# Kernel optimization log

Hardware: AMD Instinct MI355X
Metric: run time of the kernel (lower is better)

## Reference

```python
import jax, jax.numpy as jnp
import numpy as np

B, S, D = 4, 2048, 1024
H, DQK, DV = 16, 20, 64
DLQ, DLKV = 256, 128
EPS = 1e-6
NEG = -1e9


def _rms(x, w, eps=EPS):
    return x * jax.lax.rsqrt(jnp.mean(x * x, axis=-1, keepdims=True) + eps) * w


def setup_inputs() -> dict:
    key = jax.random.key(0)
    ks = jax.random.split(key, 12)
    sd = lambda n: 1.0 / np.sqrt(n)
    inp = {
        'h': jax.random.normal(ks[0], (B, S, D), jnp.float32),
        'mask': jnp.where(jnp.tril(jnp.ones((S, S), bool)), 0.0, NEG).astype(jnp.float32),
        'wq_a_w': jax.random.normal(ks[1], (DLQ, D), jnp.float32) * sd(D),
        'wq_a_b': jnp.zeros((DLQ,), jnp.float32),
        'q_norm_w': jnp.ones((DLQ,), jnp.float32),
        'wq_b_w': jax.random.normal(ks[2], (H * DQK, DLQ), jnp.float32) * sd(DLQ),
        'wq_b_b': jnp.zeros((H * DQK,), jnp.float32),
        'wkv_a_w': jax.random.normal(ks[3], (DLKV, D), jnp.float32) * sd(D),
        'wkv_a_b': jnp.zeros((DLKV,), jnp.float32),
        'kv_norm_w': jnp.ones((DLKV,), jnp.float32),
        'wkv_b_w': jax.random.normal(ks[4], (H * (DQK + DV), DLKV), jnp.float32) * sd(DLKV),
        'wo_w': jax.random.normal(ks[5], (D, H * DV), jnp.float32) * sd(H * DV),
        'wo_b': jnp.zeros((D,), jnp.float32),
    }
    return inp


def reference(h, mask, wq_a_w, wq_a_b, q_norm_w, wq_b_w, wq_b_b,
              wkv_a_w, wkv_a_b, kv_norm_w, wkv_b_w, wo_w, wo_b):
    b, s, _ = h.shape
    # query path: wq_b(q_norm(wq_a(h)))
    q_lat = _rms(h @ wq_a_w.T + wq_a_b, q_norm_w)
    q = (q_lat @ wq_b_w.T + wq_b_b).reshape(b, s, H, DQK)
    # latent kv (prefill, start_pos=0 => cache[:end_pos] == kv_norm of this chunk)
    kvn = _rms(h @ wkv_a_w.T + wkv_a_b, kv_norm_w)  # [b, t, c]
    wkv_b = wkv_b_w.reshape(H, DQK + DV, DLKV)
    # absorbed QK: project query into latent space
    q_kv = jnp.einsum('bshq,hqc->bshc', q, wkv_b[:, :DQK])
    scores = jnp.einsum('bshc,btc->bsht', q_kv, kvn) * (DQK ** -0.5)
    scores = scores + mask[:, None, :]  # causal, broadcast over heads
    p = jax.nn.softmax(scores, axis=-1).astype(h.dtype)
    v_lat = jnp.einsum('bsht,btc->bshc', p, kvn)
    v = jnp.einsum('bshc,hvc->bshv', v_lat, wkv_b[:, DQK:])
    return v.reshape(b, s, H * DV) @ wo_w.T + wo_b
```

## Files before the change

### kernel.cpp

```cpp
#include <hip/hip_runtime.h>
#include <stdint.h>

#define NB 4
#define SEQ 2048
#define DM 1024
#define NH 16
#define NDQK 20
#define NDV 64
#define DLQ 256
#define DLKV 128
#define MR (NB*SEQ)
#define NKV (NH*DLKV)

typedef __attribute__((ext_vector_type(8))) short bf8;
typedef __attribute__((ext_vector_type(4))) float f4;
typedef __attribute__((ext_vector_type(4))) short s4;

#define MFMA16(a,b,c) __builtin_amdgcn_mfma_f32_16x16x32_bf16(a, b, c, 0, 0, 0)

__device__ __forceinline__ short f2b(float f) {
  union { float f; unsigned u; } v; v.f = f;
  return (short)((v.u + 0x7FFFu + ((v.u >> 16) & 1u)) >> 16);
}

__device__ __forceinline__ void gld16(void* lds, const void* g) {
  __builtin_amdgcn_global_load_lds((const __attribute__((address_space(1))) void*)g,
                                   (__attribute__((address_space(3))) void*)lds, 16, 0, 0);
}

__global__ __launch_bounds__(256) void k_conv(const float* __restrict__ h,
    const float* __restrict__ wqa, const float* __restrict__ wkva,
    short* __restrict__ hb, short* __restrict__ wqab, short* __restrict__ wkvab) {
  const int NH4 = (MR*DM)/4, NQ4 = (DLQ*DM)/4, NK4 = (DLKV*DM)/4;
  int stride = gridDim.x * blockDim.x;
  for (int i = blockIdx.x*blockDim.x + threadIdx.x; i < NH4+NQ4+NK4; i += stride) {
    const float4* s; short* d; int o;
    if (i < NH4)            { s = (const float4*)h;    d = hb;     o = i; }
    else if (i < NH4+NQ4)   { s = (const float4*)wqa;  d = wqab;   o = i - NH4; }
    else                    { s = (const float4*)wkva; d = wkvab;  o = i - NH4 - NQ4; }
    float4 v = s[o];
    s4 r; r.x = f2b(v.x); r.y = f2b(v.y); r.z = f2b(v.z); r.w = f2b(v.w);
    *(s4*)(d + (size_t)o*4) = r;
  }
}

__global__ __launch_bounds__(256) void k_wcomb(const float* __restrict__ wqbw,
    const float* __restrict__ wqbb, const float* __restrict__ wkvb,
    short* __restrict__ Wc, float* __restrict__ bc) {
  const float SC = 0.22360679774997896f * 1.4426950408889634f;
  int n = blockIdx.x, l = threadIdx.x;
  int hh = n >> 7, c = n & 127;
  float acc = 0.f, bacc = 0.f;
  for (int q = 0; q < NDQK; ++q) {
    float wv = wkvb[(hh*84 + q)*128 + c];
    acc  += wqbw[(hh*20 + q)*256 + l] * wv;
    bacc += wqbb[hh*20 + q] * wv;
  }
  Wc[(size_t)n*256 + l] = f2b(acc * SC);
  if (l == 0) bc[n] = bacc * SC;
}

__global__ __launch_bounds__(256) void k_w2(const float* __restrict__ wo,
    const float* __restrict__ wkvb, short* __restrict__ W2) {
  int idx = blockIdx.x*256 + threadIdx.x;
  int d = idx >> 11, k = idx & 2047, hh = k >> 7, c = k & 127;
  float acc = 0.f;
  #pragma unroll 8
  for (int v = 0; v < NDV; ++v)
    acc += wo[d*1024 + hh*64 + v] * wkvb[(hh*84 + 20 + v)*128 + c];
  W2[idx] = f2b(acc);
}

template<int BN, bool WT>
__global__ __launch_bounds__(256) void k_proj_rms(const short* __restrict__ Ab,
    const short* __restrict__ Wb, const float* __restrict__ bias,
    const float* __restrict__ nw, short* __restrict__ outp, short* __restrict__ outT) {
  constexpr int WN = BN/4, NI = WN/16;
  __shared__ __align__(16) char As[32*128];
  __shared__ __align__(16) char Ws[BN*128];
  __shared__ float red[32][4];
  const int tid = threadIdx.x, l = tid & 63, w = tid >> 6;
  const int l15 = l & 15, l4 = l >> 4, l7 = l & 7, l3 = l >> 3;
  const int m0 = blockIdx.x * 32;
  f4 z = {0.f,0.f,0.f,0.f};
  f4 acc[2][NI];
  for (int mi=0;mi<2;mi++) for (int ni=0;ni<NI;ni++) acc[mi][ni] = z;
  for (int kt = 0; kt < DM/64; ++kt) {
    __syncthreads();
    { int row = w*8 + l3;
      gld16(As + w*1024 + l*16,
            (const char*)Ab + ((size_t)(m0+row)*DM + kt*64)*2 + ((l7 ^ (row&7))*16)); }
    #pragma unroll
    for (int i = 0; i < BN/32; ++i) {
      int ci = w*(BN/32) + i, row = ci*8 + l3;
      gld16(Ws + ci*1024 + l*16,
            (const char*)Wb + ((size_t)row*DM + kt*64)*2 + ((l7 ^ (row&7))*16));
    }
    asm volatile("s_waitcnt vmcnt(0)" ::: "memory");
    __syncthreads();
    #pragma unroll
    for (int kk = 0; kk < 2; ++kk) {
      bf8 a[2], bb[NI];
      #pragma unroll
      for (int mi=0;mi<2;mi++) { int row = mi*16 + l15;
        a[mi] = *(const bf8*)(As + row*128 + ((kk*64 + l4*16) ^ ((row&7)<<4))); }
      #pragma unroll
      for (int ni=0;ni<NI;ni++) { int n = w*WN + ni*16 + l15;
        bb[ni] = *(const bf8*)(Ws + n*128 + ((kk*64 + l4*16) ^ ((n&7)<<4))); }
      #pragma unroll
      for (int mi=0;mi<2;mi++)
        #pragma unroll
        for (int ni=0;ni<NI;ni++) acc[mi][ni] = MFMA16(a[mi], bb[ni], acc[mi][ni]);
    }
  }
  float bn[NI], nwv[NI];
  #pragma unroll
  for (int ni=0;ni<NI;ni++) { int n = w*WN + ni*16 + l15; bn[ni] = bias[n]; nwv[ni] = nw[n]; }
  #pragma unroll
  for (int mi=0;mi<2;mi++) {
    f4 v = z;
    #pragma unroll
    for (int ni=0;ni<NI;ni++)
      #pragma unroll
      for (int r=0;r<4;r++) { acc[mi][ni][r] += bn[ni]; v[r] += acc[mi][ni][r]*acc[mi][ni][r]; }
    #pragma unroll
    for (int r=0;r<4;r++)
      for (int x=1;x<16;x<<=1) v[r] += __shfl_xor(v[r], x);
    if (l15 == 0) {
      #pragma unroll
      for (int r=0;r<4;r++) red[mi*16 + l4*4 + r][w] = v[r];
    }
  }
  __syncthreads();
  #pragma unroll
  for (int mi=0;mi<2;mi++) {
    float sc[4];
    #pragma unroll
    for (int r=0;r<4;r++) { int row = mi*16 + l4*4 + r;
      float t = red[row][0] + red[row][1] + red[row][2] + red[row][3];
      sc[r] = rsqrtf(t * (1.0f/BN) + 1e-6f); }
    #pragma unroll
    for (int ni=0;ni<NI;ni++) { int n = w*WN + ni*16 + l15;
      #pragma unroll
      for (int r=0;r<4;r++) {
        int m = m0 + mi*16 + l4*4 + r;
        short bv = f2b(acc[mi][ni][r] * sc[r] * nwv[ni]);
        outp[(size_t)m*BN + n] = bv;
        if (WT) { int bb2 = m >> 11, s = m & 2047;
                  outT[((size_t)bb2*DLKV + n)*SEQ + s] = bv; }
      }
    }
  }
}

template<bool BOUT>
__global__ __launch_bounds__(256) void k_gemm(const short* __restrict__ A,
    const short* __restrict__ W, const float* __restrict__ bias,
    void* __restrict__ outp, int N, int K) {
  __shared__ __align__(16) char As[128*128];
  __shared__ __align__(16) char Ws[128*128];
  const int tid = threadIdx.x, l = tid & 63, w = tid >> 6;
  const int l15 = l&15, l4 = l>>4, l7 = l&7, l3 = l>>3;
  const int wm = w >> 1, wn = w & 1;
  const int n0 = blockIdx.x * 128, m0 = blockIdx.y * 128;
  f4 z = {0.f,0.f,0.f,0.f};
  f4 acc[4][4];
  for (int mi=0;mi<4;mi++) for (int ni=0;ni<4;ni++) acc[mi][ni] = z;
  for (int kt = 0; kt < (K>>6); ++kt) {
    __syncthreads();
    #pragma unroll
    for (int i=0;i<4;i++) {
      int ci = w*4 + i, row = ci*8 + l3;
      gld16(As + ci*1024 + l*16,
            (const char*)A + ((size_t)(m0+row)*K + kt*64)*2 + ((l7^(row&7))*16));
      gld16(Ws + ci*1024 + l*16,
            (const char*)W + ((size_t)(n0+row)*K + kt*64)*2 + ((l7^(row&7))*16));
    }
    asm volatile("s_waitcnt vmcnt(0)" ::: "memory");
    __syncthreads();
    #pragma unroll
    for (int kk=0;kk<2;kk++) {
      bf8 a[4], bb[4];
      #pragma unroll
      for (int mi=0;mi<4;mi++) { int row = wm*64+mi*16+l15;
        a[mi] = *(const bf8*)(As + row*128 + ((kk*64+l4*16)^((row&7)<<4))); }
      #pragma unroll
      for (int ni=0;ni<4;ni++) { int row = wn*64+ni*16+l15;
        bb[ni] = *(const bf8*)(Ws + row*128 + ((kk*64+l4*16)^((row&7)<<4))); }
      #pragma unroll
      for (int mi=0;mi<4;mi++)
        #pragma unroll
        for (int ni=0;ni<4;ni++) acc[mi][ni] = MFMA16(a[mi], bb[ni], acc[mi][ni]);
    }
  }
  #pragma unroll
  for (int ni=0;ni<4;ni++) {
    int n = n0 + wn*64 + ni*16 + l15;
    float bn = bias[n];
    #pragma unroll
    for (int mi=0;mi<4;mi++)
      #pragma unroll
      for (int r=0;r<4;r++) {
        int m = m0 + wm*64 + mi*16 + l4*4 + r;
        float val = acc[mi][ni][r] + bn;
        if (BOUT) ((short*)outp)[(size_t)m*N + n] = f2b(val);
        else      ((float*)outp)[(size_t)m*N + n] = val;
      }
  }
}

__global__ __launch_bounds__(64, 2) void k_flash(const short* __restrict__ qkv,
    const short* __restrict__ kvn, const short* __restrict__ kvnT,
    short* __restrict__ vlat) {
  __shared__ __align__(16) short Pl[32*72];
  const int l = threadIdx.x & 63;
  const int l15 = l & 15, l4 = l >> 4;
  const int hb = blockIdx.x, hh = hb & 15, b = hb >> 4;
  const int qb = 63 - (int)blockIdx.y;
  const int qw = qb * 32;
  const size_t rowbase = (size_t)(b*SEQ + qw);
  const short* Kbase = kvn  + (size_t)b*SEQ*DLKV;
  const short* Vbase = kvnT + (size_t)b*DLKV*SEQ;

  bf8 qf[2][4];
  #pragma unroll
  for (int mi=0;mi<2;mi++)
    #pragma unroll
    for (int kk=0;kk<4;kk++)
      qf[mi][kk] = *(const bf8*)(qkv + (rowbase + mi*16 + l15)*NKV + hh*128 + kk*32 + l4*8);

  f4 z = {0.f,0.f,0.f,0.f};
  f4 acc[2][8], sums[2]; float mr[2][4];
  #pragma unroll
  for (int mi=0;mi<2;mi++) { sums[mi] = z;
    #pragma unroll
    for (int cf=0;cf<8;cf++) acc[mi][cf] = z;
    #pragma unroll
    for (int r=0;r<4;r++) mr[mi][r] = -3.0e38f; }

  const short ONE = 0x3F80;
  bf8 ones; 
  #pragma unroll
  for (int j=0;j<8;j++) ones[j] = ONE;

  const int nt = ((qw + 31) >> 6) + 1;
  for (int it = 0; it < nt; ++it) {
    const int t0 = it*64;
    f4 sc[2][4];
    #pragma unroll
    for (int mi=0;mi<2;mi++)
      #pragma unroll
      for (int tf=0;tf<4;tf++) sc[mi][tf] = z;
    #pragma unroll
    for (int kk=0;kk<4;kk++) {
      bf8 bk[4];
      #pragma unroll
      for (int tf=0;tf<4;tf++)
        bk[tf] = *(const bf8*)(Kbase + (size_t)(t0 + tf*16 + l15)*DLKV + kk*32 + l4*8);
      #pragma unroll
      for (int mi=0;mi<2;mi++)
        #pragma unroll
        for (int tf=0;tf<4;tf++) sc[mi][tf] = MFMA16(qf[mi][kk], bk[tf], sc[mi][tf]);
    }
    if (t0 + 63 > qw) {
      #pragma unroll
      for (int mi=0;mi<2;mi++)
        #pragma unroll
        for (int tf=0;tf<4;tf++)
          #pragma unroll
          for (int r=0;r<4;r++) {
            int qg = qw + mi*16 + l4*4 + r, tg = t0 + tf*16 + l15;
            if (tg > qg) sc[mi][tf][r] = -3.0e38f;
          }
    }
    #pragma unroll
    for (int mi=0;mi<2;mi++) {
      float mn[4], al[4];
      #pragma unroll
      for (int r=0;r<4;r++) {
        float v = fmaxf(fmaxf(sc[mi][0][r], sc[mi][1][r]), fmaxf(sc[mi][2][r], sc[mi][3][r]));
        for (int x=1;x<16;x<<=1) v = fmaxf(v, __shfl_xor(v, x));
        float m2 = fmaxf(mr[mi][r], v);
        al[r] = exp2f(mr[mi][r] - m2);
        mr[mi][r] = m2; mn[r] = m2;
      }
      #pragma unroll
      for (int r=0;r<4;r++) { sums[mi][r] *= al[r];
        #pragma unroll
        for (int cf=0;cf<8;cf++) acc[mi][cf][r] *= al[r]; }
      #pragma unroll
      for (int tf=0;tf<4;tf++)
        #pragma unroll
        for (int r=0;r<4;r++)
          Pl[(mi*16 + l4*4 + r)*72 + tf*16 + l15] = f2b(exp2f(sc[mi][tf][r] - mn[r]));
    }
    #pragma unroll
    for (int kk=0;kk<2;kk++) {
      bf8 pa[2];
      #pragma unroll
      for (int mi=0;mi<2;mi++)
        pa[mi] = *(const bf8*)(Pl + (mi*16 + l15)*72 + kk*32 + l4*8);
      #pragma unroll
      for (int mi=0;mi<2;mi++) sums[mi] = MFMA16(pa[mi], ones, sums[mi]);
      #pragma unroll
      for (int cf=0;cf<8;cf++) {
        bf8 bv = *(const bf8*)(Vbase + (size_t)(cf*16 + l15)*SEQ + t0 + kk*32 + l4*8);
        #pragma unroll
        for (int mi=0;mi<2;mi++) acc[mi][cf] = MFMA16(pa[mi], bv, acc[mi][cf]);
      }
    }
  }
  #pragma unroll
  for (int mi=0;mi<2;mi++) {
    float inv[4];
    #pragma unroll
    for (int r=0;r<4;r++) inv[r] = 1.0f / sums[mi][r];
    #pragma unroll
    for (int cf=0;cf<8;cf++)
      #pragma unroll
      for (int r=0;r<4;r++) {
        size_t m = rowbase + mi*16 + l4*4 + r;
        vlat[m*NKV + hh*128 + cf*16 + l15] = f2b(acc[mi][cf][r] * inv[r]);
      }
  }
}

extern "C" void kernel_launch(void* const* d_in, const int* in_sizes, int n_in,
                              void* d_out, int out_size, void* d_ws, size_t ws_size,
                              hipStream_t stream) {
  const float* h     = (const float*)d_in[0];
  const float* wqaw  = (const float*)d_in[2];
  const float* wqa_b = (const float*)d_in[3];
  const float* qnw   = (const float*)d_in[4];
  const float* wqbw  = (const float*)d_in[5];
  const float* wqbb  = (const float*)d_in[6];
  const float* wkvaw = (const float*)d_in[7];
  const float* wkva_b= (const float*)d_in[8];
  const float* kvnw  = (const float*)d_in[9];
  const float* wkvb  = (const float*)d_in[10];
  const float* wow   = (const float*)d_in[11];
  const float* wob   = (const float*)d_in[12];

  char* ws = (char*)d_ws;
  size_t off = 0;
  auto alloc = [&](size_t bytes) { char* p = ws + off; off += (bytes + 255) & ~(size_t)255; return p; };
  short* hb     = (short*)alloc((size_t)MR*DM*2);
  short* wqab16 = (short*)alloc((size_t)DLQ*DM*2);
  short* wkvab16= (short*)alloc((size_t)DLKV*DM*2);
  short* qlat   = (short*)alloc((size_t)MR*DLQ*2);
  short* kvnb   = (short*)alloc((size_t)MR*DLKV*2);
  short* kvnT   = (short*)alloc((size_t)MR*DLKV*2);
  short* Wc     = (short*)alloc((size_t)NKV*DLQ*2);
  float* bc     = (float*)alloc((size_t)NKV*4);
  short* qkv    = (short*)alloc((size_t)MR*NKV*2);
  short* vlat   = (short*)alloc((size_t)MR*NKV*2);
  short* W2     = (short*)alloc((size_t)DM*NKV*2);

  k_conv<<<2048, 256, 0, stream>>>(h, wqaw, wkvaw, hb, wqab16, wkvab16);
  k_wcomb<<<NKV, 256, 0, stream>>>(wqbw, wqbb, wkvb, Wc, bc);
  k_w2<<<(DM*NKV)/256, 256, 0, stream>>>(wow, wkvb, W2);
  k_proj_rms<DLQ,  false><<<MR/32, 256, 0, stream>>>(hb, wqab16,  wqa_b,  qnw,  qlat, nullptr);
  k_proj_rms<DLKV, true ><<<MR/32, 256, 0, stream>>>(hb, wkvab16, wkva_b, kvnw, kvnb, kvnT);
  k_gemm<true ><<<dim3(NKV/128, MR/128), 256, 0, stream>>>(qlat, Wc, bc, qkv, NKV, DLQ);
  k_flash<<<dim3(64, 64), 64, 0, stream>>>(qkv, kvnb, kvnT, vlat);
  k_gemm<false><<<dim3(DM/128, MR/128), 256, 0, stream>>>(vlat, W2, wob, d_out, DM, NKV);
}
```

Baseline: 497.8 us.

## Restructure flash kernel: 8 heads per block share LDS K tiles, paired causal blocks

The flash-attention kernel now runs 8 waves per block, one per head, and all of them share one K tile of the latent KV. That tile is double-buffered in swizzled LDS through global_load_lds. Each block handles a short and a long causal query block (y and 63-y) back to back to balance work, and launches a flat grid of 256 blocks. It also prefetches V rows into registers ahead of the PV MFMAs and swaps the shuffle max reduction for DPP row operations. The aim is to cut redundant global K reads across heads and reduce load imbalance, at the cost of block-wide barriers and one block per CU.

```diff
diff --git a/kernel.cpp b/kernel.cpp
--- a/kernel.cpp
+++ b/kernel.cpp
@@ -26,6 +26,15 @@
 __device__ __forceinline__ void gld16(void* lds, const void* g) {
   __builtin_amdgcn_global_load_lds((const __attribute__((address_space(1))) void*)g,
                                    (__attribute__((address_space(3))) void*)lds, 16, 0, 0);
+}
+
+__device__ __forceinline__ float dppmax16(float v) {
+  int t;
+  t = __builtin_amdgcn_update_dpp(0, __float_as_int(v), 0xB1,  0xF, 0xF, true); v = fmaxf(v, __int_as_float(t));
+  t = __builtin_amdgcn_update_dpp(0, __float_as_int(v), 0x4E,  0xF, 0xF, true); v = fmaxf(v, __int_as_float(t));
+  t = __builtin_amdgcn_update_dpp(0, __float_as_int(v), 0x141, 0xF, 0xF, true); v = fmaxf(v, __int_as_float(t));
+  t = __builtin_amdgcn_update_dpp(0, __float_as_int(v), 0x140, 0xF, 0xF, true); v = fmaxf(v, __int_as_float(t));
+  return v;
 }
 
 __global__ __launch_bounds__(256) void k_conv(const float* __restrict__ h,
@@ -209,43 +218,65 @@
   }
 }
 
-__global__ __launch_bounds__(64, 2) void k_flash(const short* __restrict__ qkv,
+__global__ __launch_bounds__(512, 1) void k_flash(const short* __restrict__ qkv,
     const short* __restrict__ kvn, const short* __restrict__ kvnT,
     short* __restrict__ vlat) {
-  __shared__ __align__(16) short Pl[32*72];
-  const int l = threadIdx.x & 63;
+  __shared__ __align__(16) char Ks[2][64*256];
+  __shared__ __align__(16) short Pl[8][32*72];
+  const int tid = threadIdx.x, l = tid & 63, w = tid >> 6;
   const int l15 = l & 15, l4 = l >> 4;
-  const int hb = blockIdx.x, hh = hb & 15, b = hb >> 4;
-  const int qb = 63 - (int)blockIdx.y;
-  const int qw = qb * 32;
-  const size_t rowbase = (size_t)(b*SEQ + qw);
-  const short* Kbase = kvn  + (size_t)b*SEQ*DLKV;
-  const short* Vbase = kvnT + (size_t)b*DLKV*SEQ;
-
+  const int id = blockIdx.x;
+  const int b   = (id & 7) >> 1;
+  const int hh  = (((id >> 3) & 1) << 3) | w;
+  const int y   = ((id >> 4) << 1) | (id & 1);
+  const int qbs0 = y, qbs1 = 63 - y;
+  const int ntA = (y >> 1) + 1, ntT = 33;
+  const short* Kb = kvn  + (size_t)b*SEQ*DLKV;
+  const short* Vb = kvnT + (size_t)b*DLKV*SEQ;
+  short* Pw = Pl[w];
+
+  const short ONE = 0x3F80;
+  bf8 ones;
+  #pragma unroll
+  for (int j2=0;j2<8;j2++) ones[j2] = ONE;
+  f4 z = {0.f,0.f,0.f,0.f};
+
+  int qw = qbs0*32;
+  size_t rowbase = (size_t)b*SEQ + qw;
   bf8 qf[2][4];
-  #pragma unroll
-  for (int mi=0;mi<2;mi++)
+  f4 acc[2][8], sums[2]; float mr[2][4];
+  #pragma unroll
+  for (int mi=0;mi<2;mi++) {
     #pragma unroll
     for (int kk=0;kk<4;kk++)
       qf[mi][kk] = *(const bf8*)(qkv + (rowbase + mi*16 + l15)*NKV + hh*128 + kk*32 + l4*8);
-
-  f4 z = {0.f,0.f,0.f,0.f};
-  f4 acc[2][8], sums[2]; float mr[2][4];
-  #pragma unroll
-  for (int mi=0;mi<2;mi++) { sums[mi] = z;
+    sums[mi] = z;
     #pragma unroll
     for (int cf=0;cf<8;cf++) acc[mi][cf] = z;
     #pragma unroll
-    for (int r=0;r<4;r++) mr[mi][r] = -3.0e38f; }
-
-  const short ONE = 0x3F80;
-  bf8 ones; 
-  #pragma unroll
-  for (int j=0;j<8;j++) ones[j] = ONE;
-
-  const int nt = ((qw + 31) >> 6) + 1;
-  for (int it = 0; it < nt; ++it) {
-    const int t0 = it*64;
+    for (int r=0;r<4;r++) mr[mi][r] = -3.0e38f;
+  }
+
+  #pragma unroll
+  for (int r=0;r<2;r++) {
+    int ci = r*512 + tid, row = ci >> 4, c16 = ci & 15;
+    gld16(Ks[0] + ci*16, (const char*)Kb + row*256 + ((c16 ^ (row & 7))*16));
+  }
+  int cur = 0, t = 0;
+  for (int j = 0; j < ntT; ++j) {
+    const int tn = (j+1 >= ntT) ? t : ((j+1 == ntA) ? 0 : t+1);
+    {
+      const char* src = (const char*)(Kb + (size_t)tn*64*DLKV);
+      #pragma unroll
+      for (int r=0;r<2;r++) {
+        int ci = r*512 + tid, row = ci >> 4, c16 = ci & 15;
+        gld16(Ks[cur^1] + ci*16, src + row*256 + ((c16 ^ (row & 7))*16));
+      }
+    }
+    asm volatile("s_waitcnt vmcnt(2)" ::: "memory");
+    __syncthreads();
+    const int t0 = t*64;
+    const char* kb = Ks[cur];
     f4 sc[2][4];
     #pragma unroll
     for (int mi=0;mi<2;mi++)
@@ -255,13 +286,17 @@
     for (int kk=0;kk<4;kk++) {
       bf8 bk[4];
       #pragma unroll
-      for (int tf=0;tf<4;tf++)
-        bk[tf] = *(const bf8*)(Kbase + (size_t)(t0 + tf*16 + l15)*DLKV + kk*32 + l4*8);
+      for (int tf=0;tf<4;tf++) { int tt = tf*16 + l15;
+        bk[tf] = *(const bf8*)(kb + tt*256 + ((kk*64 + l4*16) ^ ((tt&7)<<4))); }
       #pragma unroll
       for (int mi=0;mi<2;mi++)
         #pragma unroll
         for (int tf=0;tf<4;tf++) sc[mi][tf] = MFMA16(qf[mi][kk], bk[tf], sc[mi][tf]);
     }
+    bf8 vr0[8], vr1[8];
+    #pragma unroll
+    for (int cf=0;cf<8;cf++)
+      vr0[cf] = *(const bf8*)(Vb + (size_t)(cf*16 + l15)*SEQ + t0 + l4*8);
     if (t0 + 63 > qw) {
       #pragma unroll
       for (int mi=0;mi<2;mi++)
@@ -279,7 +314,7 @@
       #pragma unroll
       for (int r=0;r<4;r++) {
         float v = fmaxf(fmaxf(sc[mi][0][r], sc[mi][1][r]), fmaxf(sc[mi][2][r], sc[mi][3][r]));
-        for (int x=1;x<16;x<<=1) v = fmaxf(v, __shfl_xor(v, x));
+        v = dppmax16(v);
         float m2 = fmaxf(mr[mi][r], v);
         al[r] = exp2f(mr[mi][r] - m2);
         mr[mi][r] = m2; mn[r] = m2;
@@ -292,36 +327,58 @@
       for (int tf=0;tf<4;tf++)
         #pragma unroll
         for (int r=0;r<4;r++)
-          Pl[(mi*16 + l4*4 + r)*72 + tf*16 + l15] = f2b(exp2f(sc[mi][tf][r] - mn[r]));
-    }
+          Pw[(mi*16 + l4*4 + r)*72 + tf*16 + l15] = f2b(exp2f(sc[mi][tf][r] - mn[r]));
+    }
+    #pragma unroll
+    for (int cf=0;cf<8;cf++)
+      vr1[cf] = *(const bf8*)(Vb + (size_t)(cf*16 + l15)*SEQ + t0 + 32 + l4*8);
     #pragma unroll
     for (int kk=0;kk<2;kk++) {
       bf8 pa[2];
       #pragma unroll
       for (int mi=0;mi<2;mi++)
-        pa[mi] = *(const bf8*)(Pl + (mi*16 + l15)*72 + kk*32 + l4*8);
+        pa[mi] = *(const bf8*)(Pw + (mi*16 + l15)*72 + kk*32 + l4*8);
       #pragma unroll
       for (int mi=0;mi<2;mi++) sums[mi] = MFMA16(pa[mi], ones, sums[mi]);
       #pragma unroll
       for (int cf=0;cf<8;cf++) {
-        bf8 bv = *(const bf8*)(Vbase + (size_t)(cf*16 + l15)*SEQ + t0 + kk*32 + l4*8);
+        bf8 bv = kk ? vr1[cf] : vr0[cf];
         #pragma unroll
         for (int mi=0;mi<2;mi++) acc[mi][cf] = MFMA16(pa[mi], bv, acc[mi][cf]);
       }
     }
-  }
-  #pragma unroll
-  for (int mi=0;mi<2;mi++) {
-    float inv[4];
-    #pragma unroll
-    for (int r=0;r<4;r++) inv[r] = 1.0f / sums[mi][r];
-    #pragma unroll
-    for (int cf=0;cf<8;cf++)
-      #pragma unroll
-      for (int r=0;r<4;r++) {
-        size_t m = rowbase + mi*16 + l4*4 + r;
-        vlat[m*NKV + hh*128 + cf*16 + l15] = f2b(acc[mi][cf][r] * inv[r]);
-      }
+    __syncthreads();
+    cur ^= 1;
+    if (j+1 == ntA || j+1 == ntT) {
+      #pragma unroll
+      for (int mi=0;mi<2;mi++) {
+        float inv[4];
+        #pragma unroll
+        for (int r=0;r<4;r++) inv[r] = 1.0f / sums[mi][r];
+        #pragma unroll
+        for (int cf=0;cf<8;cf++)
+          #pragma unroll
+          for (int r=0;r<4;r++) {
+            size_t m = rowbase + mi*16 + l4*4 + r;
+            vlat[m*NKV + hh*128 + cf*16 + l15] = f2b(acc[mi][cf][r] * inv[r]);
+          }
+      }
+      if (j+1 == ntA) {
+        qw = qbs1*32; rowbase = (size_t)b*SEQ + qw;
+        #pragma unroll
+        for (int mi=0;mi<2;mi++) {
+          #pragma unroll
+          for (int kk=0;kk<4;kk++)
+            qf[mi][kk] = *(const bf8*)(qkv + (rowbase + mi*16 + l15)*NKV + hh*128 + kk*32 + l4*8);
+          sums[mi] = z;
+          #pragma unroll
+          for (int cf=0;cf<8;cf++) acc[mi][cf] = z;
+          #pragma unroll
+          for (int r=0;r<4;r++) mr[mi][r] = -3.0e38f;
+        }
+      }
+    }
+    t = tn;
   }
 }
 
@@ -362,6 +419,6 @@
   k_proj_rms<DLQ,  false><<<MR/32, 256, 0, stream>>>(hb, wqab16,  wqa_b,  qnw,  qlat, nullptr);
   k_proj_rms<DLKV, true ><<<MR/32, 256, 0, stream>>>(hb, wkvab16, wkva_b, kvnw, kvnb, kvnT);
   k_gemm<true ><<<dim3(NKV/128, MR/128), 256, 0, stream>>>(qlat, Wc, bc, qkv, NKV, DLQ);
-  k_flash<<<dim3(64, 64), 64, 0, stream>>>(qkv, kvnb, kvnT, vlat);
+  k_flash<<<256, 512, 0, stream>>>(qkv, kvnb, kvnT, vlat);
   k_gemm<false><<<dim3(DM/128, MR/128), 256, 0, stream>>>(vlat, W2, wob, d_out, DM, NKV);
 }
```

Measured after the change: 413.0 us. 17.0% less time.
